# Kernel optimization log

Measured on AMD Instinct MI355X. Metric: run time of the kernel, lower is better.

Reference implementation:

```python
import jax, jax.numpy as jnp
import numpy as np

DIM = 33
EPS = 1e-5

def _conv(x, w, b, stride, pad):
    y = jax.lax.conv_general_dilated(x, w, (stride, stride), [(pad, pad), (pad, pad)],
                                     dimension_numbers=('NCHW', 'OIHW', 'NCHW'))
    return y + b[None, :, None, None]

def _lrelu(x):
    return jnp.where(x >= 0, x, 0.2 * x)

def _inorm(x, g, b):
    m = x.mean(axis=(2, 3), keepdims=True)
    v = x.var(axis=(2, 3), keepdims=True)
    return (x - m) * jax.lax.rsqrt(v + EPS) * g[None, :, None, None] + b[None, :, None, None]

def _classifier(img, w1, b1, g1, be1, w2, b2, g2, be2, w3, b3, g3, be3,
                w4, b4, g4, be4, w5, b5, w6, b6):
    x = jax.image.resize(img, (img.shape[0], 3, 256, 256), method='bilinear')
    x = _inorm(_lrelu(_conv(x, w1, b1, 2, 1)), g1, be1)   # [B,16,128,128]
    x = _inorm(_lrelu(_conv(x, w2, b2, 2, 1)), g2, be2)   # [B,32,64,64]
    x = _inorm(_lrelu(_conv(x, w3, b3, 2, 1)), g3, be3)   # [B,64,32,32]
    x = _inorm(_lrelu(_conv(x, w4, b4, 2, 1)), g4, be4)   # [B,128,16,16]
    x = _lrelu(_conv(x, w5, b5, 2, 1))                     # [B,128,8,8]
    x = _conv(x, w6, b6, 1, 0)                             # [B,3,1,1]
    return x.reshape(-1)                                   # squeeze (B=1) -> [3]

def _trilinear(lut, img):
    # lut: [3, dim, dim, dim] indexed [c, b_idx, g_idx, r_idx]; img: [B,3,H,W] in [0,1]
    scale = DIM - 1
    x = img * scale
    idx = jnp.clip(jnp.floor(x), 0, DIM - 2).astype(jnp.int32)
    f = x - idx                                            # fractional weights (differentiable in img)
    ir, ig, ib = idx[:, 0], idx[:, 1], idx[:, 2]           # [B,H,W]
    fr, fg, fb = f[:, 0], f[:, 1], f[:, 2]
    out = jnp.zeros((3,) + ir.shape, dtype=img.dtype)
    for db in (0, 1):
        wb = fb if db else 1.0 - fb
        for dg in (0, 1):
            wg = fg if dg else 1.0 - fg
            for dr in (0, 1):
                wr = fr if dr else 1.0 - fr
                corner = lut[:, ib + db, ig + dg, ir + dr]  # [3,B,H,W] gather
                out = out + (wb * wg * wr)[None] * corner
    return jnp.transpose(out, (1, 0, 2, 3))                # [B,3,H,W]

def _forward(image_input, lut0, lut1, lut2, w1, b1, g1, be1, w2, b2, g2, be2,
             w3, b3, g3, be3, w4, b4, g4, be4, w5, b5, w6, b6):
    pred = _classifier(image_input, w1, b1, g1, be1, w2, b2, g2, be2, w3, b3, g3, be3,
                       w4, b4, g4, be4, w5, b5, w6, b6)
    final_lut = pred[0] * lut0 + pred[1] * lut1 + pred[2] * lut2
    return _trilinear(final_lut, image_input)

def setup_inputs() -> dict:
    key = jax.random.key(0)
    ks = jax.random.split(key, 16)
    B, H, W = 1, 2160, 3840
    d = {}
    d['image_input'] = jax.random.uniform(ks[0], (B, 3, H, W), dtype=jnp.float32)
    d['lut0'] = jax.random.normal(ks[1], (3, DIM, DIM, DIM), dtype=jnp.float32)
    d['lut1'] = jax.random.normal(ks[2], (3, DIM, DIM, DIM), dtype=jnp.float32)
    d['lut2'] = jax.random.normal(ks[3], (3, DIM, DIM, DIM), dtype=jnp.float32)
    s = 0.05
    d['w1'] = jax.random.normal(ks[4], (16, 3, 3, 3), dtype=jnp.float32) * s
    d['b1'] = jnp.zeros((16,), jnp.float32); d['g1'] = jnp.ones((16,), jnp.float32); d['be1'] = jnp.zeros((16,), jnp.float32)
    d['w2'] = jax.random.normal(ks[5], (32, 16, 3, 3), dtype=jnp.float32) * s
    d['b2'] = jnp.zeros((32,), jnp.float32); d['g2'] = jnp.ones((32,), jnp.float32); d['be2'] = jnp.zeros((32,), jnp.float32)
    d['w3'] = jax.random.normal(ks[6], (64, 32, 3, 3), dtype=jnp.float32) * s
    d['b3'] = jnp.zeros((64,), jnp.float32); d['g3'] = jnp.ones((64,), jnp.float32); d['be3'] = jnp.zeros((64,), jnp.float32)
    d['w4'] = jax.random.normal(ks[7], (128, 64, 3, 3), dtype=jnp.float32) * s
    d['b4'] = jnp.zeros((128,), jnp.float32); d['g4'] = jnp.ones((128,), jnp.float32); d['be4'] = jnp.zeros((128,), jnp.float32)
    d['w5'] = jax.random.normal(ks[8], (128, 128, 3, 3), dtype=jnp.float32) * s
    d['b5'] = jnp.zeros((128,), jnp.float32)
    d['w6'] = jax.random.normal(ks[9], (3, 128, 8, 8), dtype=jnp.float32) * s
    d['b6'] = jnp.zeros((3,), jnp.float32)
    return d

def reference(image_input, lut0, lut1, lut2, w1, b1, g1, be1, w2, b2, g2, be2,
              w3, b3, g3, be3, w4, b4, g4, be4, w5, b5, w6, b6):
    return _forward(image_input, lut0, lut1, lut2, w1, b1, g1, be1, w2, b2, g2, be2,
                    w3, b3, g3, be3, w4, b4, g4, be4, w5, b5, w6, b6)
```

## Files before the change

### kernel.cpp

```cpp
#include <hip/hip_runtime.h>

#define NPX (2160*3840)
#define EPS 1e-5f

typedef float __attribute__((ext_vector_type(4))) fx4;

__global__ __launch_bounds__(256) void resize_w_kernel(const float* __restrict__ img,
                                                       float* __restrict__ tmp) {
  __shared__ __align__(16) float row[3872];
  const int bh = blockIdx.x;
  const float* src = img + (size_t)bh * 3840;
  const int tid = threadIdx.x;
  if (tid < 16) { row[tid] = 0.f; row[3856 + tid] = 0.f; }
  const float4* s4 = (const float4*)src;
  float4* r4 = (float4*)(row + 16);
  for (int i = tid; i < 960; i += 256) r4[i] = s4[i];
  __syncthreads();
  const int i = tid;
  const float* rp = row + 15*i + 9;
  float acc = 0.f;
  #pragma unroll
  for (int k = 0; k < 29; ++k) {
    const float w = (float)(15 - (k < 14 ? 14 - k : k - 14));
    acc = fmaf(w, rp[k], acc);
  }
  const float rcpw = (i == 0 || i == 255) ? (1.f/197.f) : (1.f/225.f);
  tmp[bh*256 + i] = acc * rcpw;
}

__global__ __launch_bounds__(256) void resize_h_kernel(const float* __restrict__ tmp,
                                                       float* __restrict__ dst) {
  const int c = blockIdx.x >> 8;
  const int oh = blockIdx.x & 255;
  const int ow = threadIdx.x;
  const float sf = ((float)oh + 0.5f) * 8.4375f - 0.5f;
  int lo = (int)ceilf(sf - 8.4375f); if (lo < 0) lo = 0;
  int hi = (int)floorf(sf + 8.4375f); if (hi > 2159) hi = 2159;
  float acc = 0.f, wsum = 0.f;
  for (int j = lo; j <= hi; ++j) {
    const float w = 1.f - fabsf(sf - (float)j) * (16.f/135.f);
    acc = fmaf(w, tmp[(c*2160 + j)*256 + ow], acc);
    wsum += w;
  }
  dst[blockIdx.x*256 + ow] = acc / wsum;
}

template<int CIN,int CICHUNK,int HIN,int WIN,int HOUT,int WOUT,int TH,int NPIN,int MODE>
__global__ __launch_bounds__(256) void conv_fused(
    const float* __restrict__ in, const float* __restrict__ wt, const float* __restrict__ bias,
    const float* __restrict__ pin, const float* __restrict__ gin, const float* __restrict__ bin,
    float* __restrict__ out, float* __restrict__ pout,
    const float* __restrict__ gself, const float* __restrict__ bself) {
  constexpr int NTW = WOUT/16;
  constexpr int NT  = (HOUT/TH)*NTW;
  constexpr int NCHUNK = CIN/CICHUNK;
  constexpr int HROWS = 2*TH + 1;
  constexpr int SLOTS = CICHUNK*HROWS*9;
  constexpr float PHW_INV = 1.f/(float)(HIN*WIN);

  __shared__ float sx[CICHUNK*HROWS*36];
  __shared__ float wl[CIN*9];
  __shared__ float sA[CIN], sB[CIN];
  __shared__ float2 wred[4];

  const int co = blockIdx.x / NT;
  const int t  = blockIdx.x % NT;
  const int oh0 = (t / NTW)*TH, ow0 = (t % NTW)*16;
  const int tid = threadIdx.x;

  for (int i = tid; i < CIN*9; i += 256) wl[i] = wt[co*CIN*9 + i];
  if (NPIN > 0) {
    if (tid < CIN) {
      const float2* p2 = (const float2*)pin;
      float s = 0.f, q = 0.f;
      #pragma unroll 4
      for (int k = 0; k < NPIN; ++k) { float2 p = p2[tid*NPIN + k]; s += p.x; q += p.y; }
      const float m = s * PHW_INV;
      float var = q * PHW_INV - m*m; var = fmaxf(var, 0.f);
      const float A = gin[tid] * rsqrtf(var + EPS);
      sA[tid] = A; sB[tid] = bin[tid] - m*A;
    }
  }
  __syncthreads();

  const int ohl = tid >> 4, owl = tid & 15;
  const bool active = (ohl < TH);
  float acc = bias[co];

  for (int cc = 0; cc < NCHUNK; ++cc) {
    if (cc) __syncthreads();
    const int cb = cc*CICHUNK;
    for (int i = tid; i < SLOTS; i += 256) {
      const int ci_l = i / (HROWS*9);
      const int rem  = i - ci_l*(HROWS*9);
      const int r = rem / 9, q = rem - r*9;
      const int grow = 2*oh0 - 1 + r;
      const int ga   = 2*ow0 - 4 + 4*q;
      float4 v = make_float4(0.f,0.f,0.f,0.f);
      if (grow >= 0 && grow < HIN && ga >= 0) {
        v = *(const float4*)(in + ((size_t)(cb+ci_l)*HIN + grow)*WIN + ga);
        if (NPIN > 0) {
          const float A = sA[cb+ci_l], B = sB[cb+ci_l];
          v.x = fmaf(A, v.x, B); v.y = fmaf(A, v.y, B);
          v.z = fmaf(A, v.z, B); v.w = fmaf(A, v.w, B);
        }
      }
      *(float4*)&sx[(ci_l*HROWS + r)*36 + q*4] = v;
    }
    __syncthreads();
    if (active) {
      #pragma unroll 4
      for (int ci_l = 0; ci_l < CICHUNK; ++ci_l) {
        const float* sp = sx + ci_l*(HROWS*36);
        const float* wp = wl + (cb+ci_l)*9;
        #pragma unroll
        for (int kh = 0; kh < 3; ++kh) {
          const float* rp = sp + (2*ohl + kh)*36 + 3 + 2*owl;
          acc = fmaf(rp[0], wp[kh*3+0], acc);
          acc = fmaf(rp[1], wp[kh*3+1], acc);
          acc = fmaf(rp[2], wp[kh*3+2], acc);
        }
      }
    }
  }

  acc = acc >= 0.f ? acc : 0.2f*acc;
  if (active) out[(size_t)co*HOUT*WOUT + (oh0+ohl)*WOUT + ow0 + owl] = acc;

  float s = active ? acc : 0.f;
  float q = active ? acc*acc : 0.f;
  #pragma unroll
  for (int off = 32; off > 0; off >>= 1) {
    s += __shfl_down(s, off);
    q += __shfl_down(q, off);
  }
  if ((tid & 63) == 0) wred[tid >> 6] = make_float2(s, q);
  __syncthreads();
  if (tid == 0) {
    const float S = wred[0].x + wred[1].x + wred[2].x + wred[3].x;
    const float Q = wred[0].y + wred[1].y + wred[2].y + wred[3].y;
    if (MODE == 1) {
      ((float2*)pout)[co*NT + t] = make_float2(S, Q);
    } else {
      const float m = S / (float)(HOUT*WOUT);
      float var = Q / (float)(HOUT*WOUT) - m*m; var = fmaxf(var, 0.f);
      const float A = gself[co] * rsqrtf(var + EPS);
      pout[co*2]   = A;
      pout[co*2+1] = bself[co] - m*A;
    }
  }
}

__global__ __launch_bounds__(256) void conv5_fused(const float* __restrict__ in,
    const float* __restrict__ wt, const float* __restrict__ bias,
    const float* __restrict__ pin, const float* __restrict__ gin, const float* __restrict__ bin,
    const float* __restrict__ w6, float* __restrict__ part) {
  __shared__ float sx[32*17*20];
  __shared__ float wl[128*9];
  __shared__ float sA[128], sB[128];
  __shared__ float red[256];
  const int co = blockIdx.x;
  const int tid = threadIdx.x;
  for (int i = tid; i < 1152; i += 256) wl[i] = wt[co*1152 + i];
  if (tid < 128) {
    const float2* p2 = (const float2*)pin;
    const float2 pa = p2[tid*2], pb = p2[tid*2+1];
    const float m = (pa.x + pb.x) * (1.f/256.f);
    float var = (pa.y + pb.y) * (1.f/256.f) - m*m; var = fmaxf(var, 0.f);
    const float A = gin[tid] * rsqrtf(var + EPS);
    sA[tid] = A; sB[tid] = bin[tid] - m*A;
  }
  __syncthreads();

  const int px = tid & 63, q = tid >> 6;
  const int ohl = px >> 3, owl = px & 7;
  float acc = 0.f;
  for (int cc = 0; cc < 4; ++cc) {
    if (cc) __syncthreads();
    const int cb = cc*32;
    for (int i = tid; i < 32*17*5; i += 256) {
      const int ci_l = i / 85;
      const int rem  = i - ci_l*85;
      const int r = rem / 5, qq = rem - r*5;
      const int grow = r - 1;
      const int ga   = 4*qq - 4;
      float4 v = make_float4(0.f,0.f,0.f,0.f);
      if (grow >= 0 && grow < 16 && ga >= 0) {
        v = *(const float4*)(in + ((size_t)(cb+ci_l)*16 + grow)*16 + ga);
        const float A = sA[cb+ci_l], B = sB[cb+ci_l];
        v.x = fmaf(A, v.x, B); v.y = fmaf(A, v.y, B);
        v.z = fmaf(A, v.z, B); v.w = fmaf(A, v.w, B);
      }
      *(float4*)&sx[(ci_l*17 + r)*20 + qq*4] = v;
    }
    __syncthreads();
    #pragma unroll 2
    for (int k = 0; k < 8; ++k) {
      const int ci_l = q*8 + k;
      const float* sp = sx + ci_l*340;
      const float* wp = wl + (cb+ci_l)*9;
      #pragma unroll
      for (int kh = 0; kh < 3; ++kh) {
        const float* rp = sp + (2*ohl + kh)*20 + 3 + 2*owl;
        acc = fmaf(rp[0], wp[kh*3+0], acc);
        acc = fmaf(rp[1], wp[kh*3+1], acc);
        acc = fmaf(rp[2], wp[kh*3+2], acc);
      }
    }
  }
  red[tid] = acc;
  __syncthreads();
  if (tid < 64) {
    float a = red[tid] + red[tid+64] + red[tid+128] + red[tid+192] + bias[co];
    a = a >= 0.f ? a : 0.2f*a;
    #pragma unroll
    for (int j = 0; j < 3; ++j) {
      float v = a * w6[(j*128 + co)*64 + tid];
      #pragma unroll
      for (int off = 32; off > 0; off >>= 1) v += __shfl_down(v, off);
      if (tid == 0) part[co*3 + j] = v;
    }
  }
}

__global__ __launch_bounds__(256) void blend_pack_kernel(const float* __restrict__ l0,
    const float* __restrict__ l1, const float* __restrict__ l2,
    const float* __restrict__ part, const float* __restrict__ b6,
    unsigned* __restrict__ flp) {
  __shared__ float sred[2][3];
  __shared__ float sp[3];
  const int tid = threadIdx.x;
  float a0 = 0.f, a1 = 0.f, a2 = 0.f;
  if (tid < 128) { a0 = part[tid*3]; a1 = part[tid*3+1]; a2 = part[tid*3+2]; }
  #pragma unroll
  for (int off = 32; off > 0; off >>= 1) {
    a0 += __shfl_down(a0, off);
    a1 += __shfl_down(a1, off);
    a2 += __shfl_down(a2, off);
  }
  if (tid < 128 && (tid & 63) == 0) {
    sred[tid >> 6][0] = a0; sred[tid >> 6][1] = a1; sred[tid >> 6][2] = a2;
  }
  __syncthreads();
  if (tid < 3) sp[tid] = sred[0][tid] + sred[1][tid] + b6[tid];
  __syncthreads();
  const int i = blockIdx.x*256 + tid;
  if (i >= 3*35936) return;
  const int c = i / 35936, j = i - c*35936;
  const int src = c*35937 + j;
  const float v0 = sp[0]*l0[src]   + sp[1]*l1[src]   + sp[2]*l2[src];
  const float v1 = sp[0]*l0[src+1] + sp[1]*l1[src+1] + sp[2]*l2[src+1];
  unsigned u0 = __float_as_uint(v0); u0 = (u0 + 0x7fffu + ((u0>>16)&1u)) >> 16;
  unsigned u1 = __float_as_uint(v1); u1 = (u1 + 0x7fffu + ((u1>>16)&1u)) >> 16;
  flp[c*35936 + j] = u0 | (u1 << 16);
}

__global__ __launch_bounds__(1024, 4) void trilinear_kernel(const float* __restrict__ img,
    const unsigned* __restrict__ flp, float* __restrict__ out) {
  __shared__ unsigned slut[35936];
  const int tid = threadIdx.x;
  const int chunk = blockIdx.x / 3;
  const int c     = blockIdx.x % 3;
  {
    uint4* d4 = (uint4*)slut;
    const uint4* s4 = (const uint4*)(flp + c*35936);
    for (int i = tid; i < 8984; i += 1024) d4[i] = s4[i];
  }
  __syncthreads();
  const int p0 = chunk * 32400;
  const float* imR = img + p0;
  const float* imG = img + NPX + p0;
  const float* imB = img + 2*NPX + p0;
  float* op = out + (size_t)c*NPX + p0;
  for (int g = tid; g < 4050; g += 1024) {
    const int pA = 4*g;
    const int pB = pA + 16200;
    float rv[8], gv[8], bv[8], ov[8];
    {
      const float4 A = *(const float4*)(imR + pA);
      const float4 B = *(const float4*)(imR + pB);
      rv[0]=A.x; rv[1]=A.y; rv[2]=A.z; rv[3]=A.w;
      rv[4]=B.x; rv[5]=B.y; rv[6]=B.z; rv[7]=B.w;
    }
    {
      const float4 A = *(const float4*)(imG + pA);
      const float4 B = *(const float4*)(imG + pB);
      gv[0]=A.x; gv[1]=A.y; gv[2]=A.z; gv[3]=A.w;
      gv[4]=B.x; gv[5]=B.y; gv[6]=B.z; gv[7]=B.w;
    }
    {
      const float4 A = *(const float4*)(imB + pA);
      const float4 B = *(const float4*)(imB + pB);
      bv[0]=A.x; bv[1]=A.y; bv[2]=A.z; bv[3]=A.w;
      bv[4]=B.x; bv[5]=B.y; bv[6]=B.z; bv[7]=B.w;
    }
    #pragma unroll
    for (int k = 0; k < 8; ++k) {
      const float xr = rv[k]*32.f, xg = gv[k]*32.f, xb = bv[k]*32.f;
      const int ir = (int)xr, ig = (int)xg, ib = (int)xb;
      const float fr = xr - (float)ir;
      const float fg = xg - (float)ig;
      const float fb = xb - (float)ib;
      const int base = (ib*33 + ig)*33 + ir;
      const unsigned p00 = slut[base],      p01 = slut[base+33];
      const unsigned p10 = slut[base+1089], p11 = slut[base+1122];
      const float v000 = __uint_as_float(p00 << 16), v001 = __uint_as_float(p00 & 0xffff0000u);
      const float v010 = __uint_as_float(p01 << 16), v011 = __uint_as_float(p01 & 0xffff0000u);
      const float v100 = __uint_as_float(p10 << 16), v101 = __uint_as_float(p10 & 0xffff0000u);
      const float v110 = __uint_as_float(p11 << 16), v111 = __uint_as_float(p11 & 0xffff0000u);
      const float a0 = fmaf(fr, v001 - v000, v000);
      const float a1 = fmaf(fr, v011 - v010, v010);
      const float a2 = fmaf(fr, v101 - v100, v100);
      const float a3 = fmaf(fr, v111 - v110, v110);
      const float lo = fmaf(fg, a1 - a0, a0);
      const float hi = fmaf(fg, a3 - a2, a2);
      ov[k] = fmaf(fb, hi - lo, lo);
    }
    fx4 r0 = {ov[0], ov[1], ov[2], ov[3]};
    fx4 r1 = {ov[4], ov[5], ov[6], ov[7]};
    __builtin_nontemporal_store(r0, (fx4*)(op + pA));
    __builtin_nontemporal_store(r1, (fx4*)(op + pB));
  }
}

extern "C" void kernel_launch(void* const* d_in, const int* in_sizes, int n_in,
                              void* d_out, int out_size, void* d_ws, size_t ws_size,
                              hipStream_t stream) {
  const float* img  = (const float*)d_in[0];
  const float* lut0 = (const float*)d_in[1];
  const float* lut1 = (const float*)d_in[2];
  const float* lut2 = (const float*)d_in[3];
  const float* w1 = (const float*)d_in[4];  const float* b1  = (const float*)d_in[5];
  const float* g1 = (const float*)d_in[6];  const float* be1 = (const float*)d_in[7];
  const float* w2 = (const float*)d_in[8];  const float* b2  = (const float*)d_in[9];
  const float* g2 = (const float*)d_in[10]; const float* be2 = (const float*)d_in[11];
  const float* w3 = (const float*)d_in[12]; const float* b3  = (const float*)d_in[13];
  const float* g3 = (const float*)d_in[14]; const float* be3 = (const float*)d_in[15];
  const float* w4 = (const float*)d_in[16]; const float* b4  = (const float*)d_in[17];
  const float* g4 = (const float*)d_in[18]; const float* be4 = (const float*)d_in[19];
  const float* w5 = (const float*)d_in[20]; const float* b5  = (const float*)d_in[21];
  const float* w6 = (const float*)d_in[22]; const float* b6  = (const float*)d_in[23];

  float* ws = (float*)d_ws;
  float* tmp   = ws;
  float* r256  = ws + 1658880;
  float* c1    = ws;
  float* c2    = ws + 262144;
  float* c3    = ws + 393216;
  float* c4    = ws + 458752;
  float* part1 = ws + 491520;
  float* part2 = ws + 493568;
  float* part3 = ws + 494592;
  float* part4 = ws + 495104;
  float* part6 = ws + 495616;
  unsigned* flp = (unsigned*)(ws + 496128);

  resize_w_kernel<<<3*2160, 256, 0, stream>>>(img, tmp);
  resize_h_kernel<<<3*256, 256, 0, stream>>>(tmp, r256);

  conv_fused< 3, 3,256,256,128,128,16, 0,1><<<16*64, 256, 0, stream>>>(
      r256, w1, b1, nullptr, nullptr, nullptr, c1, part1, nullptr, nullptr);
  conv_fused<16,16,128,128, 64, 64,16,64,1><<<32*16, 256, 0, stream>>>(
      c1, w2, b2, part1, g1, be1, c2, part2, nullptr, nullptr);
  conv_fused<32,32, 64, 64, 32, 32,16,16,1><<<64*4, 256, 0, stream>>>(
      c2, w3, b3, part2, g2, be2, c3, part3, nullptr, nullptr);
  conv_fused<64,32, 32, 32, 16, 16, 8, 4,1><<<128*2, 256, 0, stream>>>(
      c3, w4, b4, part3, g3, be3, c4, part4, nullptr, nullptr);
  conv5_fused<<<128, 256, 0, stream>>>(c4, w5, b5, part4, g4, be4, w6, part6);

  blend_pack_kernel<<<422, 256, 0, stream>>>(lut0, lut1, lut2, part6, b6, flp);
  trilinear_kernel<<<768, 1024, 0, stream>>>(img, flp, (float*)d_out);
}
```

Baseline: 183.0 us.

## Pack LUT as non-overlapping bf16 pairs to halve shared memory footprint

The per-channel blended LUT was stored as overlapping bf16 pairs (each word holding entries r and r+1), which doubled its size to about 140 KB of LDS. It is now packed as disjoint pairs per row of 33 entries (17 words per row), halving shared memory so more blocks can be resident, and the launch bound is raised to 8 blocks per CU. The cost is twice as many LDS reads per corner lookup, plus parity-dependent selects to extract the right halves.

```diff
diff --git a/kernel.cpp b/kernel.cpp
--- a/kernel.cpp
+++ b/kernel.cpp
@@ -245,26 +245,28 @@
   if (tid < 3) sp[tid] = sred[0][tid] + sred[1][tid] + b6[tid];
   __syncthreads();
   const int i = blockIdx.x*256 + tid;
-  if (i >= 3*35936) return;
-  const int c = i / 35936, j = i - c*35936;
-  const int src = c*35937 + j;
-  const float v0 = sp[0]*l0[src]   + sp[1]*l1[src]   + sp[2]*l2[src];
-  const float v1 = sp[0]*l0[src+1] + sp[1]*l1[src+1] + sp[2]*l2[src+1];
+  if (i >= 3*18513) return;
+  const int c = i / 18513, rem = i - c*18513;
+  const int row = rem / 17, j = rem - row*17;
+  const int src = c*35937 + row*33 + 2*j;
+  const float v0 = sp[0]*l0[src] + sp[1]*l1[src] + sp[2]*l2[src];
+  float v1 = 0.f;
+  if (2*j + 1 <= 32) v1 = sp[0]*l0[src+1] + sp[1]*l1[src+1] + sp[2]*l2[src+1];
   unsigned u0 = __float_as_uint(v0); u0 = (u0 + 0x7fffu + ((u0>>16)&1u)) >> 16;
   unsigned u1 = __float_as_uint(v1); u1 = (u1 + 0x7fffu + ((u1>>16)&1u)) >> 16;
-  flp[c*35936 + j] = u0 | (u1 << 16);
-}
-
-__global__ __launch_bounds__(1024, 4) void trilinear_kernel(const float* __restrict__ img,
+  flp[c*18516 + rem] = u0 | (u1 << 16);
+}
+
+__global__ __launch_bounds__(1024, 8) void trilinear_kernel(const float* __restrict__ img,
     const unsigned* __restrict__ flp, float* __restrict__ out) {
-  __shared__ unsigned slut[35936];
+  __shared__ unsigned slut[18516];
   const int tid = threadIdx.x;
   const int chunk = blockIdx.x / 3;
   const int c     = blockIdx.x % 3;
   {
     uint4* d4 = (uint4*)slut;
-    const uint4* s4 = (const uint4*)(flp + c*35936);
-    for (int i = tid; i < 8984; i += 1024) d4[i] = s4[i];
+    const uint4* s4 = (const uint4*)(flp + c*18516);
+    for (int i = tid; i < 4629; i += 1024) d4[i] = s4[i];
   }
   __syncthreads();
   const int p0 = chunk * 32400;
@@ -301,13 +303,22 @@
       const float fr = xr - (float)ir;
       const float fg = xg - (float)ig;
       const float fb = xb - (float)ib;
-      const int base = (ib*33 + ig)*33 + ir;
-      const unsigned p00 = slut[base],      p01 = slut[base+33];
-      const unsigned p10 = slut[base+1089], p11 = slut[base+1122];
-      const float v000 = __uint_as_float(p00 << 16), v001 = __uint_as_float(p00 & 0xffff0000u);
-      const float v010 = __uint_as_float(p01 << 16), v011 = __uint_as_float(p01 & 0xffff0000u);
-      const float v100 = __uint_as_float(p10 << 16), v101 = __uint_as_float(p10 & 0xffff0000u);
-      const float v110 = __uint_as_float(p11 << 16), v111 = __uint_as_float(p11 & 0xffff0000u);
+      const int rb = (ib*33 + ig)*17;
+      const int jA = rb + (ir >> 1);
+      const int jB = rb + ((ir + 1) >> 1);
+      const bool odd = (ir & 1) != 0;
+      const unsigned w0a = slut[jA],       w0b = slut[jB];
+      const unsigned w1a = slut[jA + 17],  w1b = slut[jB + 17];
+      const unsigned w2a = slut[jA + 561], w2b = slut[jB + 561];
+      const unsigned w3a = slut[jA + 578], w3b = slut[jB + 578];
+      const float v000 = __uint_as_float(odd ? (w0a & 0xffff0000u) : (w0a << 16));
+      const float v001 = __uint_as_float(odd ? (w0b << 16) : (w0a & 0xffff0000u));
+      const float v010 = __uint_as_float(odd ? (w1a & 0xffff0000u) : (w1a << 16));
+      const float v011 = __uint_as_float(odd ? (w1b << 16) : (w1a & 0xffff0000u));
+      const float v100 = __uint_as_float(odd ? (w2a & 0xffff0000u) : (w2a << 16));
+      const float v101 = __uint_as_float(odd ? (w2b << 16) : (w2a & 0xffff0000u));
+      const float v110 = __uint_as_float(odd ? (w3a & 0xffff0000u) : (w3a << 16));
+      const float v111 = __uint_as_float(odd ? (w3b << 16) : (w3a & 0xffff0000u));
       const float a0 = fmaf(fr, v001 - v000, v000);
       const float a1 = fmaf(fr, v011 - v010, v010);
       const float a2 = fmaf(fr, v101 - v100, v100);
@@ -368,6 +379,6 @@
       c3, w4, b4, part3, g3, be3, c4, part4, nullptr, nullptr);
   conv5_fused<<<128, 256, 0, stream>>>(c4, w5, b5, part4, g4, be4, w6, part6);
 
-  blend_pack_kernel<<<422, 256, 0, stream>>>(lut0, lut1, lut2, part6, b6, flp);
+  blend_pack_kernel<<<218, 256, 0, stream>>>(lut0, lut1, lut2, part6, b6, flp);
   trilinear_kernel<<<768, 1024, 0, stream>>>(img, flp, (float*)d_out);
 }
```

Result: faster. 177.0 us (-3.3%).
